# Performance work log

Measured on AMD Instinct MI355X. Metric: run time of the kernel, lower is better.

## Reference

```python
import jax, jax.numpy as jnp
import numpy as np

B, S, D = 8, 1024, 1024

def setup_inputs() -> dict:
    key = jax.random.key(0)
    ks = jax.random.split(key, 6)
    context = jax.random.normal(ks[0], (B, S, D), dtype=jnp.float32)
    eos_mask = jax.random.randint(ks[1], (B, S), 0, 2, dtype=jnp.int32)
    prior = jax.random.uniform(ks[2], (), dtype=jnp.float32)
    adj_mat = jax.random.randint(ks[3], (B, S, S), 0, 2, dtype=jnp.int32)
    Wk = jax.random.normal(ks[4], (D, D), dtype=jnp.float32) * 0.02
    Wq = jax.random.normal(ks[5], (D, D), dtype=jnp.float32) * 0.02
    bk = jnp.zeros((D,), jnp.float32)
    bq = jnp.zeros((D,), jnp.float32)
    ln_gamma = jnp.ones((D,), jnp.float32)
    ln_beta = jnp.zeros((D,), jnp.float32)
    return {"context": context, "eos_mask": eos_mask, "prior": prior,
            "adj_mat": adj_mat, "Wk": Wk, "bk": bk, "Wq": Wq, "bq": bq,
            "ln_gamma": ln_gamma, "ln_beta": ln_beta}

def reference(context, eos_mask, prior, adj_mat, Wk, bk, Wq, bq, ln_gamma, ln_beta):
    d_model = context.shape[-1]
    seq_len = context.shape[1]
    # LayerNorm (annotated-transformer style: unbiased std, eps added to std)
    mu = jnp.mean(context, axis=-1, keepdims=True)
    std = jnp.std(context, axis=-1, keepdims=True, ddof=1)
    x = ln_gamma * (context - mu) / (std + 1e-6) + ln_beta
    # projections (torch Linear: x @ W.T + b)
    key_p = x @ Wk.T + bk
    query = x @ Wq.T + bq
    scores = jnp.einsum('bqd,bkd->bqk', query, key_p) / (d_model / 2)
    scores = jnp.where(adj_mat == 0, -1e9, scores)
    neibor_attn = jax.nn.softmax(scores, axis=-1)
    neibor_attn = jnp.sqrt(neibor_attn * jnp.swapaxes(neibor_attn, -1, -2) + 1e-9)
    neibor_attn = prior + (1.0 - prior) * neibor_attn
    # constant structural matrices
    a = jnp.eye(seq_len, k=1, dtype=jnp.float32)          # superdiagonal
    b = jnp.eye(seq_len, dtype=jnp.float32)               # diagonal
    tri = jnp.triu(jnp.ones((seq_len, seq_len), jnp.float32))  # upper incl diag
    # t = (log(attn+eps) masked to superdiagonal) @ tri
    t = jnp.matmul(jnp.where(a == 0, 0.0, jnp.log(neibor_attn + 1e-9)), tri)
    g_attn = jnp.exp(jnp.matmul(tri, t))
    g_attn = jnp.where((tri - b) == 0, 0.0, g_attn)  # keep strict upper only
    g_attn = g_attn + jnp.swapaxes(g_attn, -1, -2) + jnp.where(b == 0, 1e-9, neibor_attn)
    return (g_attn, neibor_attn)
```

## Files before the change

### kernel.cpp

```cpp
#include <hip/hip_runtime.h>
#include <hip/hip_bf16.h>

#define S_LEN 1024
#define D_DIM 1024
#define N_BAT 8
#define BSS   (8ull*1024ull*1024ull)

using bf16x8 = __attribute__((ext_vector_type(8))) short;
using f32x4  = __attribute__((ext_vector_type(4))) float;

__device__ __forceinline__ short f2bf(float v) {
    __hip_bfloat16 h = __float2bfloat16(v);
    return *reinterpret_cast<short*>(&h);
}

__device__ __forceinline__ void gload_lds16(const void* g, void* l) {
    __builtin_amdgcn_global_load_lds(
        (const __attribute__((address_space(1))) void*)g,
        (__attribute__((address_space(3))) void*)l, 16, 0, 0);
}

__global__ __launch_bounds__(256) void ln_kernel(
    const float* __restrict__ X, const float* __restrict__ gamma,
    const float* __restrict__ beta, short* __restrict__ Y)
{
    __shared__ float sh[8];
    const size_t row = blockIdx.x;
    const int t = threadIdx.x;
    float4 v = ((const float4*)(X + row * 1024))[t];
    float s  = v.x + v.y + v.z + v.w;
    float ss = v.x*v.x + v.y*v.y + v.z*v.z + v.w*v.w;
    for (int off = 32; off > 0; off >>= 1) {
        s  += __shfl_down(s, off);
        ss += __shfl_down(ss, off);
    }
    const int lane = t & 63, w = t >> 6;
    if (lane == 0) { sh[w] = s; sh[4 + w] = ss; }
    __syncthreads();
    if (t == 0) {
        float S  = sh[0] + sh[1] + sh[2] + sh[3];
        float SS = sh[4] + sh[5] + sh[6] + sh[7];
        float mu = S * (1.0f / 1024.0f);
        float var = fmaxf((SS - S * mu) * (1.0f / 1023.0f), 0.0f);
        sh[0] = mu;
        sh[1] = 1.0f / (sqrtf(var) + 1e-6f);
    }
    __syncthreads();
    const float mu = sh[0], inv = sh[1];
    float4 g  = ((const float4*)gamma)[t];
    float4 be = ((const float4*)beta)[t];
    short4 o;
    o.x = f2bf(g.x * (v.x - mu) * inv + be.x);
    o.y = f2bf(g.y * (v.y - mu) * inv + be.y);
    o.z = f2bf(g.z * (v.z - mu) * inv + be.z);
    o.w = f2bf(g.w * (v.w - mu) * inv + be.w);
    ((short4*)(Y + row * 1024))[t] = o;
}

__global__ __launch_bounds__(256) void cvt_kernel(
    const float* __restrict__ Wk, const float* __restrict__ Wq,
    short* __restrict__ wkb, short* __restrict__ wqb)
{
    const size_t i = (size_t)blockIdx.x * 256 + threadIdx.x;
    if (i < 1024ull * 1024ull) {
        wkb[i] = f2bf(Wk[i]);
        wqb[i] = f2bf(Wq[i]);
    }
}

__global__ __launch_bounds__(256) void gemm_proj(
    const short* __restrict__ A, const short* __restrict__ Bt,
    const float* __restrict__ bias, short* __restrict__ C)
{
    __shared__ short As[128 * 32];
    __shared__ short Bs[128 * 32];
    const int tid  = threadIdx.x;
    const int lane = tid & 63;
    const int w    = tid >> 6;
    const int wr   = w >> 1, wc = w & 1;
    const int brow = blockIdx.x * 128;
    const int bcol = blockIdx.y * 128;

    f32x4 acc[4][4];
#pragma unroll
    for (int m = 0; m < 4; ++m)
#pragma unroll
        for (int n = 0; n < 4; ++n) acc[m][n] = 0.0f;

    for (int k0 = 0; k0 < 1024; k0 += 32) {
#pragma unroll
        for (int c = 0; c < 2; ++c) {
            const int base = w * 2048 + c * 1024;
            const int chunk = base + lane * 16;
            const int row = chunk >> 6;
            const int col = (chunk & 63) >> 1;
            gload_lds16(A  + (size_t)(brow + row) * 1024 + (k0 + col),
                        (char*)As + base);
            gload_lds16(Bt + (size_t)(bcol + row) * 1024 + (k0 + col),
                        (char*)Bs + base);
        }
        __syncthreads();
        bf16x8 af[4], bfr[4];
        const int rsel = lane & 15;
        const int ksel = (lane >> 4) * 8;
#pragma unroll
        for (int m = 0; m < 4; ++m)
            af[m] = *(const bf16x8*)&As[(wr * 64 + m * 16 + rsel) * 32 + ksel];
#pragma unroll
        for (int n = 0; n < 4; ++n)
            bfr[n] = *(const bf16x8*)&Bs[(wc * 64 + n * 16 + rsel) * 32 + ksel];
#pragma unroll
        for (int m = 0; m < 4; ++m)
#pragma unroll
            for (int n = 0; n < 4; ++n)
                acc[m][n] = __builtin_amdgcn_mfma_f32_16x16x32_bf16(
                    af[m], bfr[n], acc[m][n], 0, 0, 0);
        __syncthreads();
    }
#pragma unroll
    for (int m = 0; m < 4; ++m)
#pragma unroll
        for (int n = 0; n < 4; ++n) {
            const int colg = bcol + wc * 64 + n * 16 + (lane & 15);
            const float bv = bias[colg];
#pragma unroll
            for (int r = 0; r < 4; ++r) {
                const int rowg = brow + wr * 64 + m * 16 + ((lane >> 4) * 4 + r);
                C[(size_t)rowg * 1024 + colg] = f2bf(acc[m][n][r] + bv);
            }
        }
}

__global__ __launch_bounds__(256) void gemm_scores(
    const short* __restrict__ Qm, const short* __restrict__ Km,
    float* __restrict__ Sc)
{
    __shared__ short As[128 * 32];
    __shared__ short Bs[128 * 32];
    const int b = blockIdx.z;
    const short* A  = Qm + (size_t)b * 1024 * 1024;
    const short* Bt = Km + (size_t)b * 1024 * 1024;
    float* C = Sc + (size_t)b * 1024 * 1024;

    const int tid  = threadIdx.x;
    const int lane = tid & 63;
    const int w    = tid >> 6;
    const int wr   = w >> 1, wc = w & 1;
    const int brow = blockIdx.x * 128;
    const int bcol = blockIdx.y * 128;

    f32x4 acc[4][4];
#pragma unroll
    for (int m = 0; m < 4; ++m)
#pragma unroll
        for (int n = 0; n < 4; ++n) acc[m][n] = 0.0f;

    for (int k0 = 0; k0 < 1024; k0 += 32) {
#pragma unroll
        for (int c = 0; c < 2; ++c) {
            const int base = w * 2048 + c * 1024;
            const int chunk = base + lane * 16;
            const int row = chunk >> 6;
            const int col = (chunk & 63) >> 1;
            gload_lds16(A  + (size_t)(brow + row) * 1024 + (k0 + col),
                        (char*)As + base);
            gload_lds16(Bt + (size_t)(bcol + row) * 1024 + (k0 + col),
                        (char*)Bs + base);
        }
        __syncthreads();
        bf16x8 af[4], bfr[4];
        const int rsel = lane & 15;
        const int ksel = (lane >> 4) * 8;
#pragma unroll
        for (int m = 0; m < 4; ++m)
            af[m] = *(const bf16x8*)&As[(wr * 64 + m * 16 + rsel) * 32 + ksel];
#pragma unroll
        for (int n = 0; n < 4; ++n)
            bfr[n] = *(const bf16x8*)&Bs[(wc * 64 + n * 16 + rsel) * 32 + ksel];
#pragma unroll
        for (int m = 0; m < 4; ++m)
#pragma unroll
            for (int n = 0; n < 4; ++n)
                acc[m][n] = __builtin_amdgcn_mfma_f32_16x16x32_bf16(
                    af[m], bfr[n], acc[m][n], 0, 0, 0);
        __syncthreads();
    }
#pragma unroll
    for (int m = 0; m < 4; ++m)
#pragma unroll
        for (int n = 0; n < 4; ++n) {
            const int colg = bcol + wc * 64 + n * 16 + (lane & 15);
#pragma unroll
            for (int r = 0; r < 4; ++r) {
                const int rowg = brow + wr * 64 + m * 16 + ((lane >> 4) * 4 + r);
                C[(size_t)rowg * 1024 + colg] = acc[m][n][r] * 0.001953125f;
            }
        }
}

__global__ __launch_bounds__(256) void softmax_kernel(
    const float* __restrict__ Sc, const int* __restrict__ adj,
    float* __restrict__ At)
{
    __shared__ float sh[4];
    const size_t row = blockIdx.x;
    const int t = threadIdx.x;
    const float4 sv = ((const float4*)(Sc + row * 1024))[t];
    const int4   av = ((const int4*)(adj + row * 1024))[t];
    float m = -3.0e38f;
    if (av.x) m = fmaxf(m, sv.x);
    if (av.y) m = fmaxf(m, sv.y);
    if (av.z) m = fmaxf(m, sv.z);
    if (av.w) m = fmaxf(m, sv.w);
    for (int off = 32; off > 0; off >>= 1) m = fmaxf(m, __shfl_down(m, off));
    const int lane = t & 63, w = t >> 6;
    if (lane == 0) sh[w] = m;
    __syncthreads();
    const float M = fmaxf(fmaxf(sh[0], sh[1]), fmaxf(sh[2], sh[3]));
    __syncthreads();
    float e0 = av.x ? expf(sv.x - M) : 0.0f;
    float e1 = av.y ? expf(sv.y - M) : 0.0f;
    float e2 = av.z ? expf(sv.z - M) : 0.0f;
    float e3 = av.w ? expf(sv.w - M) : 0.0f;
    float s = e0 + e1 + e2 + e3;
    for (int off = 32; off > 0; off >>= 1) s += __shfl_down(s, off);
    if (lane == 0) sh[w] = s;
    __syncthreads();
    const float Sm = sh[0] + sh[1] + sh[2] + sh[3];
    float4 o;
    if (Sm > 0.0f) {
        const float inv = 1.0f / Sm;
        o.x = e0 * inv; o.y = e1 * inv; o.z = e2 * inv; o.w = e3 * inv;
    } else {
        o.x = o.y = o.z = o.w = 1.0f / 1024.0f;
    }
    ((float4*)(At + row * 1024))[t] = o;
}

__global__ __launch_bounds__(256) void na_kernel(
    float* __restrict__ At, const float* __restrict__ prior_p)
{
    const int ti = blockIdx.x >> 5, tj = blockIdx.x & 31;
    if (tj < ti) return;
    const int b = blockIdx.y;
    const float prior = *prior_p;
    const float om = 1.0f - prior;
    float* base = At + (size_t)b * 1024 * 1024;
    __shared__ float T1[32][33];
    __shared__ float T2[32][33];
    const int c = threadIdx.x & 31, r0 = threadIdx.x >> 5;
#pragma unroll
    for (int rr = 0; rr < 4; ++rr) {
        const int r = r0 + rr * 8;
        T1[r][c] = base[(size_t)(ti * 32 + r) * 1024 + tj * 32 + c];
        T2[r][c] = base[(size_t)(tj * 32 + r) * 1024 + ti * 32 + c];
    }
    __syncthreads();
#pragma unroll
    for (int rr = 0; rr < 4; ++rr) {
        const int r = r0 + rr * 8;
        const float na1 = prior + om * sqrtf(T1[r][c] * T2[c][r] + 1e-9f);
        base[(size_t)(ti * 32 + r) * 1024 + tj * 32 + c] = na1;
        const float na2 = prior + om * sqrtf(T2[r][c] * T1[c][r] + 1e-9f);
        base[(size_t)(tj * 32 + r) * 1024 + ti * 32 + c] = na2;
    }
}

__global__ __launch_bounds__(1024) void cum_kernel(
    const float* __restrict__ At, double* __restrict__ cum)
{
    __shared__ double sh[1024];
    const int b = blockIdx.x;
    const int t = threadIdx.x;
    const float* na = At + (size_t)b * 1024 * 1024;
    double v = 0.0;
    if (t >= 1) {
        const int k = t - 1;
        v = (double)logf(na[(size_t)k * 1024 + (k + 1)] + 1e-9f);
    }
    sh[t] = v;
    __syncthreads();
#pragma unroll
    for (int off = 1; off < 1024; off <<= 1) {
        const double add = (t >= off) ? sh[t - off] : 0.0;
        __syncthreads();
        sh[t] += add;
        __syncthreads();
    }
    cum[b * 1024 + t] = sh[t];
}

__global__ __launch_bounds__(256) void g_kernel(
    const float* __restrict__ At, const double* __restrict__ cum,
    float* __restrict__ G)
{
    const size_t stride = (size_t)gridDim.x * 256;
    for (size_t i = (size_t)blockIdx.x * 256 + threadIdx.x; i < BSS; i += stride) {
        const int b = (int)(i >> 20);
        const int rem = (int)(i & 1048575);
        const int r = rem >> 10, c = rem & 1023;
        float val;
        if (r == c) {
            val = At[i];
        } else {
            const int lo = min(r, c), hi = max(r, c);
            val = expf((float)(cum[b * 1024 + hi] - cum[b * 1024 + lo])) + 1e-9f;
        }
        G[i] = val;
    }
}

extern "C" void kernel_launch(void* const* d_in, const int* in_sizes, int n_in,
                              void* d_out, int out_size, void* d_ws, size_t ws_size,
                              hipStream_t stream)
{
    const float* context = (const float*)d_in[0];
    const float* prior   = (const float*)d_in[2];
    const int*   adj     = (const int*)d_in[3];
    const float* Wk      = (const float*)d_in[4];
    const float* bk      = (const float*)d_in[5];
    const float* Wq      = (const float*)d_in[6];
    const float* bq      = (const float*)d_in[7];
    const float* gamma   = (const float*)d_in[8];
    const float* beta    = (const float*)d_in[9];

    float* out   = (float*)d_out;
    float* gout  = out;
    float* naout = out + BSS;

    char* ws = (char*)d_ws;
    short*  xb   = (short*)(ws);
    short*  wkb  = (short*)(ws + (16ull << 20));
    short*  wqb  = (short*)(ws + (18ull << 20));
    short*  keyb = (short*)(ws + (20ull << 20));
    short*  qryb = (short*)(ws + (36ull << 20));
    double* cumd = (double*)(ws + (52ull << 20));

    ln_kernel<<<8192, 256, 0, stream>>>(context, gamma, beta, xb);
    cvt_kernel<<<4096, 256, 0, stream>>>(Wk, Wq, wkb, wqb);
    gemm_proj<<<dim3(64, 8), 256, 0, stream>>>(xb, wkb, bk, keyb);
    gemm_proj<<<dim3(64, 8), 256, 0, stream>>>(xb, wqb, bq, qryb);
    gemm_scores<<<dim3(8, 8, 8), 256, 0, stream>>>(qryb, keyb, gout);
    softmax_kernel<<<8192, 256, 0, stream>>>(gout, adj, naout);
    na_kernel<<<dim3(1024, 8), 256, 0, stream>>>(naout, prior);
    cum_kernel<<<8, 1024, 0, stream>>>(naout, cumd);
    g_kernel<<<8192, 256, 0, stream>>>(naout, cumd, gout);
}
```

Before: 148.3 us.

## Fold Wq^T Wk into one matrix and fuse neighbor-attn with g computation

Rewrites scores as x (Wq^T Wk) x^T plus rank-one bias terms, so the two 8192x1024x1024 projections become one small 1024^3 weight GEMM plus one activation GEMM. The bias contributions are precomputed as vectors (u, v, c0) and dotted inside LayerNorm. It also computes the superdiagonal neighbor values directly from the softmax output in the scan kernel. This lets the symmetric sqrt pass and the G fill be fused into one tiled kernel, removing a full extra pass over the 8x1024x1024 buffers. The risk is extra bf16 rounding from the combined weight matrix and the intermediate T.

```diff
diff --git a/kernel.cpp b/kernel.cpp
--- a/kernel.cpp
+++ b/kernel.cpp
@@ -20,11 +20,40 @@
         (__attribute__((address_space(3))) void*)l, 16, 0, 0);
 }
 
+__global__ __launch_bounds__(256) void bias_vec_kernel(
+    const float* __restrict__ Wq, const float* __restrict__ Wk,
+    const float* __restrict__ bk, const float* __restrict__ bq,
+    float* __restrict__ u, float* __restrict__ v, float* __restrict__ c0)
+{
+    __shared__ float sh[4];
+    const int i = blockIdx.x * 256 + threadIdx.x;
+    float au = 0.0f, av = 0.0f;
+    for (int j = 0; j < 1024; ++j) {
+        au += Wq[(size_t)j * 1024 + i] * bk[j];
+        av += Wk[(size_t)j * 1024 + i] * bq[j];
+    }
+    u[i] = au;
+    v[i] = av;
+    if (blockIdx.x == 0) {
+        const int t = threadIdx.x;
+        float4 a = ((const float4*)bq)[t];
+        float4 b = ((const float4*)bk)[t];
+        float s = a.x*b.x + a.y*b.y + a.z*b.z + a.w*b.w;
+        for (int off = 32; off > 0; off >>= 1) s += __shfl_down(s, off);
+        const int lane = t & 63, w = t >> 6;
+        if (lane == 0) sh[w] = s;
+        __syncthreads();
+        if (t == 0) c0[0] = sh[0] + sh[1] + sh[2] + sh[3];
+    }
+}
+
 __global__ __launch_bounds__(256) void ln_kernel(
     const float* __restrict__ X, const float* __restrict__ gamma,
-    const float* __restrict__ beta, short* __restrict__ Y)
-{
-    __shared__ float sh[8];
+    const float* __restrict__ beta, const float* __restrict__ u,
+    const float* __restrict__ v2, short* __restrict__ Y,
+    float* __restrict__ p, float* __restrict__ r2)
+{
+    __shared__ float sh[16];
     const size_t row = blockIdx.x;
     const int t = threadIdx.x;
     float4 v = ((const float4*)(X + row * 1024))[t];
@@ -49,26 +78,52 @@
     const float mu = sh[0], inv = sh[1];
     float4 g  = ((const float4*)gamma)[t];
     float4 be = ((const float4*)beta)[t];
+    float y0 = g.x * (v.x - mu) * inv + be.x;
+    float y1 = g.y * (v.y - mu) * inv + be.y;
+    float y2 = g.z * (v.z - mu) * inv + be.z;
+    float y3 = g.w * (v.w - mu) * inv + be.w;
     short4 o;
-    o.x = f2bf(g.x * (v.x - mu) * inv + be.x);
-    o.y = f2bf(g.y * (v.y - mu) * inv + be.y);
-    o.z = f2bf(g.z * (v.z - mu) * inv + be.z);
-    o.w = f2bf(g.w * (v.w - mu) * inv + be.w);
+    o.x = f2bf(y0); o.y = f2bf(y1); o.z = f2bf(y2); o.w = f2bf(y3);
     ((short4*)(Y + row * 1024))[t] = o;
-}
-
-__global__ __launch_bounds__(256) void cvt_kernel(
-    const float* __restrict__ Wk, const float* __restrict__ Wq,
-    short* __restrict__ wkb, short* __restrict__ wqb)
-{
-    const size_t i = (size_t)blockIdx.x * 256 + threadIdx.x;
-    if (i < 1024ull * 1024ull) {
-        wkb[i] = f2bf(Wk[i]);
-        wqb[i] = f2bf(Wq[i]);
-    }
-}
-
-__global__ __launch_bounds__(256) void gemm_proj(
+    float4 uu = ((const float4*)u)[t];
+    float4 vv = ((const float4*)v2)[t];
+    float dp = y0*uu.x + y1*uu.y + y2*uu.z + y3*uu.w;
+    float dr = y0*vv.x + y1*vv.y + y2*vv.z + y3*vv.w;
+    for (int off = 32; off > 0; off >>= 1) {
+        dp += __shfl_down(dp, off);
+        dr += __shfl_down(dr, off);
+    }
+    if (lane == 0) { sh[8 + w] = dp; sh[12 + w] = dr; }
+    __syncthreads();
+    if (t == 0) {
+        p[row]  = sh[8] + sh[9] + sh[10] + sh[11];
+        r2[row] = sh[12] + sh[13] + sh[14] + sh[15];
+    }
+}
+
+__global__ __launch_bounds__(256) void cvt_t_kernel(
+    const float* __restrict__ Wq, const float* __restrict__ Wk,
+    short* __restrict__ wqt, short* __restrict__ wkt)
+{
+    __shared__ float T[32][33];
+    const float* src = blockIdx.z ? Wk : Wq;
+    short* dst = blockIdx.z ? wkt : wqt;
+    const int bi = blockIdx.x * 32, bj = blockIdx.y * 32;
+    const int c = threadIdx.x & 31, r0 = threadIdx.x >> 5;
+#pragma unroll
+    for (int rr = 0; rr < 4; ++rr) {
+        const int r = r0 + rr * 8;
+        T[r][c] = src[(size_t)(bi + r) * 1024 + bj + c];
+    }
+    __syncthreads();
+#pragma unroll
+    for (int rr = 0; rr < 4; ++rr) {
+        const int r = r0 + rr * 8;
+        dst[(size_t)(bj + r) * 1024 + bi + c] = f2bf(T[c][r]);
+    }
+}
+
+__global__ __launch_bounds__(256) void gemm_bf16(
     const short* __restrict__ A, const short* __restrict__ Bt,
     const float* __restrict__ bias, short* __restrict__ C)
 {
@@ -122,7 +177,7 @@
 #pragma unroll
         for (int n = 0; n < 4; ++n) {
             const int colg = bcol + wc * 64 + n * 16 + (lane & 15);
-            const float bv = bias[colg];
+            const float bv = bias ? bias[colg] : 0.0f;
 #pragma unroll
             for (int r = 0; r < 4; ++r) {
                 const int rowg = brow + wr * 64 + m * 16 + ((lane >> 4) * 4 + r);
@@ -132,14 +187,17 @@
 }
 
 __global__ __launch_bounds__(256) void gemm_scores(
-    const short* __restrict__ Qm, const short* __restrict__ Km,
-    float* __restrict__ Sc)
+    const short* __restrict__ Tm, const short* __restrict__ Xm,
+    const float* __restrict__ p, const float* __restrict__ r2,
+    const float* __restrict__ c0p, float* __restrict__ Sc)
 {
     __shared__ short As[128 * 32];
     __shared__ short Bs[128 * 32];
     const int b = blockIdx.z;
-    const short* A  = Qm + (size_t)b * 1024 * 1024;
-    const short* Bt = Km + (size_t)b * 1024 * 1024;
+    const short* A  = Tm + (size_t)b * 1024 * 1024;
+    const short* Bt = Xm + (size_t)b * 1024 * 1024;
+    const float* pb = p  + (size_t)b * 1024;
+    const float* rb = r2 + (size_t)b * 1024;
     float* C = Sc + (size_t)b * 1024 * 1024;
 
     const int tid  = threadIdx.x;
@@ -185,15 +243,18 @@
                     af[m], bfr[n], acc[m][n], 0, 0, 0);
         __syncthreads();
     }
+    const float c0v = c0p[0];
 #pragma unroll
     for (int m = 0; m < 4; ++m)
 #pragma unroll
         for (int n = 0; n < 4; ++n) {
             const int colg = bcol + wc * 64 + n * 16 + (lane & 15);
+            const float radd = rb[colg] + c0v;
 #pragma unroll
             for (int r = 0; r < 4; ++r) {
                 const int rowg = brow + wr * 64 + m * 16 + ((lane >> 4) * 4 + r);
-                C[(size_t)rowg * 1024 + colg] = acc[m][n][r] * 0.001953125f;
+                C[(size_t)rowg * 1024 + colg] =
+                    (acc[m][n][r] + pb[rowg] + radd) * 0.001953125f;
             }
         }
 }
@@ -237,8 +298,39 @@
     ((float4*)(At + row * 1024))[t] = o;
 }
 
-__global__ __launch_bounds__(256) void na_kernel(
-    float* __restrict__ At, const float* __restrict__ prior_p)
+__global__ __launch_bounds__(1024) void cum2_kernel(
+    const float* __restrict__ At, const float* __restrict__ prior_p,
+    double* __restrict__ cum)
+{
+    __shared__ double sh[1024];
+    const int b = blockIdx.x;
+    const int t = threadIdx.x;
+    const float prior = *prior_p;
+    const float om = 1.0f - prior;
+    const float* attn = At + (size_t)b * 1024 * 1024;
+    double v = 0.0;
+    if (t >= 1) {
+        const int k = t - 1;
+        const float a1 = attn[(size_t)k * 1024 + (k + 1)];
+        const float a2 = attn[(size_t)(k + 1) * 1024 + k];
+        const float na = prior + om * sqrtf(a1 * a2 + 1e-9f);
+        v = (double)logf(na + 1e-9f);
+    }
+    sh[t] = v;
+    __syncthreads();
+#pragma unroll
+    for (int off = 1; off < 1024; off <<= 1) {
+        const double add = (t >= off) ? sh[t - off] : 0.0;
+        __syncthreads();
+        sh[t] += add;
+        __syncthreads();
+    }
+    cum[b * 1024 + t] = sh[t];
+}
+
+__global__ __launch_bounds__(256) void na_g_kernel(
+    float* __restrict__ At, const float* __restrict__ prior_p,
+    const double* __restrict__ cum, float* __restrict__ G)
 {
     const int ti = blockIdx.x >> 5, tj = blockIdx.x & 31;
     if (tj < ti) return;
@@ -246,6 +338,8 @@
     const float prior = *prior_p;
     const float om = 1.0f - prior;
     float* base = At + (size_t)b * 1024 * 1024;
+    float* gb   = G  + (size_t)b * 1024 * 1024;
+    const double* cb = cum + (size_t)b * 1024;
     __shared__ float T1[32][33];
     __shared__ float T2[32][33];
     const int c = threadIdx.x & 31, r0 = threadIdx.x >> 5;
@@ -259,54 +353,26 @@
 #pragma unroll
     for (int rr = 0; rr < 4; ++rr) {
         const int r = r0 + rr * 8;
+        const int R1 = ti * 32 + r, C1 = tj * 32 + c;
         const float na1 = prior + om * sqrtf(T1[r][c] * T2[c][r] + 1e-9f);
-        base[(size_t)(ti * 32 + r) * 1024 + tj * 32 + c] = na1;
+        base[(size_t)R1 * 1024 + C1] = na1;
+        float g1;
+        if (R1 == C1) g1 = na1;
+        else {
+            const int lo = min(R1, C1), hi = max(R1, C1);
+            g1 = expf((float)(cb[hi] - cb[lo])) + 1e-9f;
+        }
+        gb[(size_t)R1 * 1024 + C1] = g1;
+        const int R2 = tj * 32 + r, C2 = ti * 32 + c;
         const float na2 = prior + om * sqrtf(T2[r][c] * T1[c][r] + 1e-9f);
-        base[(size_t)(tj * 32 + r) * 1024 + ti * 32 + c] = na2;
-    }
-}
-
-__global__ __launch_bounds__(1024) void cum_kernel(
-    const float* __restrict__ At, double* __restrict__ cum)
-{
-    __shared__ double sh[1024];
-    const int b = blockIdx.x;
-    const int t = threadIdx.x;
-    const float* na = At + (size_t)b * 1024 * 1024;
-    double v = 0.0;
-    if (t >= 1) {
-        const int k = t - 1;
-        v = (double)logf(na[(size_t)k * 1024 + (k + 1)] + 1e-9f);
-    }
-    sh[t] = v;
-    __syncthreads();
-#pragma unroll
-    for (int off = 1; off < 1024; off <<= 1) {
-        const double add = (t >= off) ? sh[t - off] : 0.0;
-        __syncthreads();
-        sh[t] += add;
-        __syncthreads();
-    }
-    cum[b * 1024 + t] = sh[t];
-}
-
-__global__ __launch_bounds__(256) void g_kernel(
-    const float* __restrict__ At, const double* __restrict__ cum,
-    float* __restrict__ G)
-{
-    const size_t stride = (size_t)gridDim.x * 256;
-    for (size_t i = (size_t)blockIdx.x * 256 + threadIdx.x; i < BSS; i += stride) {
-        const int b = (int)(i >> 20);
-        const int rem = (int)(i & 1048575);
-        const int r = rem >> 10, c = rem & 1023;
-        float val;
-        if (r == c) {
-            val = At[i];
-        } else {
-            const int lo = min(r, c), hi = max(r, c);
-            val = expf((float)(cum[b * 1024 + hi] - cum[b * 1024 + lo])) + 1e-9f;
-        }
-        G[i] = val;
+        base[(size_t)R2 * 1024 + C2] = na2;
+        float g2;
+        if (R2 == C2) g2 = na2;
+        else {
+            const int lo = min(R2, C2), hi = max(R2, C2);
+            g2 = expf((float)(cb[hi] - cb[lo])) + 1e-9f;
+        }
+        gb[(size_t)R2 * 1024 + C2] = g2;
     }
 }
 
@@ -330,19 +396,25 @@
 
     char* ws = (char*)d_ws;
     short*  xb   = (short*)(ws);
-    short*  wkb  = (short*)(ws + (16ull << 20));
-    short*  wqb  = (short*)(ws + (18ull << 20));
-    short*  keyb = (short*)(ws + (20ull << 20));
-    short*  qryb = (short*)(ws + (36ull << 20));
-    double* cumd = (double*)(ws + (52ull << 20));
-
-    ln_kernel<<<8192, 256, 0, stream>>>(context, gamma, beta, xb);
-    cvt_kernel<<<4096, 256, 0, stream>>>(Wk, Wq, wkb, wqb);
-    gemm_proj<<<dim3(64, 8), 256, 0, stream>>>(xb, wkb, bk, keyb);
-    gemm_proj<<<dim3(64, 8), 256, 0, stream>>>(xb, wqb, bq, qryb);
-    gemm_scores<<<dim3(8, 8, 8), 256, 0, stream>>>(qryb, keyb, gout);
+    short*  wqt  = (short*)(ws + (16ull << 20));
+    short*  wkt  = (short*)(ws + (18ull << 20));
+    short*  m2t  = (short*)(ws + (20ull << 20));
+    short*  tb   = (short*)(ws + (22ull << 20));
+    double* cumd = (double*)(ws + (38ull << 20));
+    float*  uvec = (float*)(ws + (38ull << 20) + (1ull << 16));
+    float*  vvec = uvec + 1024;
+    float*  c0   = vvec + 1024;
+    float*  pvec = c0 + 64;
+    float*  rvec = pvec + 8192;
+
+    bias_vec_kernel<<<4, 256, 0, stream>>>(Wq, Wk, bk, bq, uvec, vvec, c0);
+    ln_kernel<<<8192, 256, 0, stream>>>(context, gamma, beta, uvec, vvec,
+                                        xb, pvec, rvec);
+    cvt_t_kernel<<<dim3(32, 32, 2), 256, 0, stream>>>(Wq, Wk, wqt, wkt);
+    gemm_bf16<<<dim3(8, 8), 256, 0, stream>>>(wkt, wqt, nullptr, m2t);
+    gemm_bf16<<<dim3(64, 8), 256, 0, stream>>>(xb, m2t, nullptr, tb);
+    gemm_scores<<<dim3(8, 8, 8), 256, 0, stream>>>(tb, xb, pvec, rvec, c0, gout);
     softmax_kernel<<<8192, 256, 0, stream>>>(gout, adj, naout);
-    na_kernel<<<dim3(1024, 8), 256, 0, stream>>>(naout, prior);
-    cum_kernel<<<8, 1024, 0, stream>>>(naout, cumd);
-    g_kernel<<<8192, 256, 0, stream>>>(naout, cumd, gout);
-}
+    cum2_kernel<<<8, 1024, 0, stream>>>(naout, prior, cumd);
+    na_g_kernel<<<dim3(1024, 8), 256, 0, stream>>>(naout, prior, cumd, gout);
+}
```

After: 207.5 us. 1.4x slower.
